# Kernel optimization log

Hardware: AMD Instinct MI355X
Metric: run time of the kernel (lower is better)

The kernel has to match this reference:

```python
import jax, jax.numpy as jnp
import numpy as np


def gat(feat_src, feat_dst, src, dst, W, al, ar, b):
    # DGL GATConv in eval mode: shared fc for src/dst, additive attention,
    # leaky_relu(0.2), edge-softmax per destination node, elu activation, bias.
    H, D = al.shape
    nd = feat_dst.shape[0]
    hs = (feat_src @ W).reshape(-1, H, D)  # [Ns,H,D]
    hd = (feat_dst @ W).reshape(-1, H, D)  # [Nd,H,D]
    el = (hs * al).sum(-1)  # [Ns,H]
    er = (hd * ar).sum(-1)  # [Nd,H]
    e = jax.nn.leaky_relu(el[src] + er[dst], 0.2)  # [E,H]
    m = jax.lax.stop_gradient(jax.ops.segment_max(e, dst, num_segments=nd))
    a = jnp.exp(e - m[dst])
    s = jax.ops.segment_sum(a, dst, num_segments=nd)
    den = s[dst]
    alpha = a / jnp.where(den == 0, 1.0, den)  # allow_zero_in_degree
    rst = jax.ops.segment_sum(alpha[:, :, None] * hs[src], dst, num_segments=nd)
    return jax.nn.elu(rst + b.reshape(H, D))  # [Nd,H,D]


def setup_inputs():
    key = jax.random.key(0)
    ks = jax.random.split(key, 40)
    NP, NQ, NK, NA = 50000, 20000, 30000, 5000
    EM, EQ, EK, EA = 1600000, 200000, 200000, 100000
    IN, ATT, HID, H, OUT = 128, 64, 32, 4, 1000
    w = lambda k, sh: jax.random.normal(k, sh, jnp.float32) * 0.05
    ri = lambda k, e, n: jax.random.randint(k, (e,), 0, n, dtype=jnp.int32)
    d = dict(
        hp=jax.random.normal(ks[0], (NP, IN), jnp.float32),
        hq=jax.random.normal(ks[1], (NQ, ATT), jnp.float32),
        hk=jax.random.normal(ks[2], (NK, ATT), jnp.float32),
        ha=jax.random.normal(ks[3], (NA, ATT), jnp.float32),
        meta_src=ri(ks[4], EM, NP), meta_dst=ri(ks[5], EM, NP),
        q_src=ri(ks[6], EQ, NQ), q_dst=ri(ks[7], EQ, NP),
        k_src=ri(ks[8], EK, NK), k_dst=ri(ks[9], EK, NP),
        a_src=ri(ks[10], EA, NA), a_dst=ri(ks[11], EA, NP),
        W0=w(ks[12], (IN, H * HID)), al0=w(ks[13], (H, HID)), ar0=w(ks[14], (H, HID)), b0=jnp.zeros((H * HID,), jnp.float32),
        W1=w(ks[15], (H * HID, H * HID)), al1=w(ks[16], (H, HID)), ar1=w(ks[17], (H, HID)), b1=jnp.zeros((H * HID,), jnp.float32),
        Wq=w(ks[18], (64, H * 128)), alq=w(ks[19], (H, 128)), arq=w(ks[20], (H, 128)), bq=jnp.zeros((H * 128,), jnp.float32),
        Wkw=w(ks[21], (64, H * 128)), alkw=w(ks[22], (H, 128)), arkw=w(ks[23], (H, 128)), bkw=jnp.zeros((H * 128,), jnp.float32),
        Watt=w(ks[24], (64, H * 128)), alatt=w(ks[25], (H, 128)), aratt=w(ks[26], (H, 128)), batt=jnp.zeros((H * 128,), jnp.float32),
        Wpnn_a=w(ks[27], (IN, 64)), Wpn_a=w(ks[28], (ATT, 64)),
        Wpnn=w(ks[29], (H * HID, 64)), Wpn=w(ks[30], (H * 128, 64)),
        Wpred=w(ks[31], (256, OUT)), bpred=jnp.zeros((OUT,), jnp.float32),
    )
    return d


def reference(hp, hq, hk, ha, meta_src, meta_dst, q_src, q_dst, k_src, k_dst, a_src, a_dst, W0, al0, ar0, b0, W1, al1, ar1, b1, Wq, alq, arq, bq, Wkw, alkw, arkw, bkw, Watt, alatt, aratt, batt, Wpnn_a, Wpn_a, Wpnn, Wpn, Wpred, bpred):
    NP = hp.shape[0]
    # two pnn_layers over the single used metapath graph (index 1 is skipped in the original)
    h = gat(hp, hp, meta_src, meta_dst, W0, al0, ar0, b0).reshape(NP, -1)  # [NP,128]
    h = gat(h, h, meta_src, meta_dst, W1, al1, ar1, b1).reshape(NP, -1)    # [NP,128]
    hpd = hp @ Wpnn_a  # proj_pnn_a(hp_cache) -> dst features for bipartite GATs
    oq = gat(hq @ Wpn_a, hpd, q_src, q_dst, Wq, alq, arq, bq).reshape(NP, -1)      # [NP,512]
    ok = gat(hk @ Wpn_a, hpd, k_src, k_dst, Wkw, alkw, arkw, bkw).reshape(NP, -1)  # [NP,512]
    oa = gat(ha @ Wpn_a, hpd, a_src, a_dst, Watt, alatt, aratt, batt).reshape(NP, -1)  # [NP,512]
    hcat = jnp.concatenate([h @ Wpnn, oq @ Wpn, ok @ Wpn, oa @ Wpn], axis=1)  # [NP,256]
    return hcat @ Wpred + bpred
```

## Files before the change

### kernel.cpp

```cpp
#include <hip/hip_runtime.h>
#include <hip/hip_bf16.h>
#include <math.h>
#include <stdint.h>

typedef __attribute__((ext_vector_type(8))) short bh8;
typedef __attribute__((ext_vector_type(4))) float f32x4;

#define AS1(p) ((const __attribute__((address_space(1))) void*)(p))
#define AS3(p) ((__attribute__((address_space(3))) void*)(p))

__device__ inline ushort f2b(float f){
  uint u = __builtin_bit_cast(uint, f);
  u += 0x7fff + ((u >> 16) & 1);
  return (ushort)(u >> 16);
}
__device__ inline float b2f(ushort b){ return __builtin_bit_cast(float, (uint)b << 16); }

__global__ void fill_zero_i32(int* __restrict__ p, int n){
  int i = blockIdx.x*blockDim.x + threadIdx.x;
  if(i < n) p[i] = 0;
}

struct P4 { const int* src; const int* dst; uint* ebuf; int E; int cap; int bbeg; int bend; };

__global__ __launch_bounds__(256) void partition_all_k(P4 g0, P4 g1, P4 g2, P4 g3,
    int* __restrict__ bcur, int range){
  P4 G; int gi;
  int b = blockIdx.x;
  if(b < g0.bend){ G = g0; gi = 0; }
  else if(b < g1.bend){ G = g1; gi = 1; }
  else if(b < g2.bend){ G = g2; gi = 2; }
  else { G = g3; gi = 3; }
  const int lb = b - G.bbeg, nb = G.bend - G.bbeg;
  __shared__ int hist[8], base[8];
  const int tid = threadIdx.x;
  int* bc = bcur + gi*8;
  for(int c0 = lb*256; c0 < G.E; c0 += nb*256){
    int i = c0 + tid;
    int d = 0, s = 0, bk = -1;
    if(i < G.E){ d = G.dst[i]; s = G.src[i]; bk = d / range; }
    if(tid < 8) hist[tid] = 0;
    __syncthreads();
    int rank = 0;
    if(bk >= 0) rank = atomicAdd(&hist[bk], 1);
    __syncthreads();
    if(tid < 8) base[tid] = hist[tid] ? atomicAdd(&bc[tid], hist[tid]) : 0;
    __syncthreads();
    if(bk >= 0){
      int pos = base[bk] + rank;
      if(pos < G.cap) G.ebuf[(size_t)bk*G.cap + pos] = ((uint)s << 13) | (uint)(d - bk*range);
    }
    __syncthreads();
  }
}

struct B4 { const uint* ebuf; int cap; int* cnt; int bbeg; int bend; };
__global__ __launch_bounds__(256) void count_all_k(B4 g0, B4 g1, B4 g2, B4 g3,
    const int* __restrict__ bcur, int range){
  B4 G; int gi;
  int b = blockIdx.x;
  if(b < g0.bend){ G = g0; gi = 0; }
  else if(b < g1.bend){ G = g1; gi = 1; }
  else if(b < g2.bend){ G = g2; gi = 2; }
  else { G = g3; gi = 3; }
  const int local = b - G.bbeg, J = (G.bend - G.bbeg) >> 3;
  const int bk = local & 7, j = local >> 3;
  int nb = bcur[gi*8 + bk]; if(nb > G.cap) nb = G.cap;
  const uint* eb = G.ebuf + (size_t)bk*G.cap;
  int* cb = G.cnt + bk*range;
  int per = (nb + J - 1)/J;
  int beg = j*per, end = beg + per; if(end > nb) end = nb;
  for(int i = beg + threadIdx.x; i < end; i += 256)
    atomicAdd(&cb[eb[i] & 8191u], 1);
}

struct SB4 { const uint* ebuf; int cap; int* cursor; int* colv; int bbeg; int bend; };
__global__ __launch_bounds__(256) void scatter_all_k(SB4 g0, SB4 g1, SB4 g2, SB4 g3,
    const int* __restrict__ bcur, int range){
  SB4 G; int gi;
  int b = blockIdx.x;
  if(b < g0.bend){ G = g0; gi = 0; }
  else if(b < g1.bend){ G = g1; gi = 1; }
  else if(b < g2.bend){ G = g2; gi = 2; }
  else { G = g3; gi = 3; }
  const int local = b - G.bbeg, J = (G.bend - G.bbeg) >> 3;
  const int bk = local & 7, j = local >> 3;
  int nb = bcur[gi*8 + bk]; if(nb > G.cap) nb = G.cap;
  const uint* eb = G.ebuf + (size_t)bk*G.cap;
  int* ub = G.cursor + bk*range;
  int per = (nb + J - 1)/J;
  int beg = j*per, end = beg + per; if(end > nb) end = nb;
  for(int i = beg + threadIdx.x; i < end; i += 256){
    uint e = eb[i];
    int p = atomicAdd(&ub[e & 8191u], 1);
    G.colv[p] = (int)(e >> 13);
  }
}

__global__ __launch_bounds__(1024) void scan4_k(
    const int* c0, const int* c1, const int* c2, const int* c3,
    int* o0, int* o1, int* o2, int* o3,
    int* u0, int* u1, int* u2, int* u3, int n){
  const int* cnt = blockIdx.x==0?c0:(blockIdx.x==1?c1:(blockIdx.x==2?c2:c3));
  int* ofs    = blockIdx.x==0?o0:(blockIdx.x==1?o1:(blockIdx.x==2?o2:o3));
  int* cursor = blockIdx.x==0?u0:(blockIdx.x==1?u1:(blockIdx.x==2?u2:u3));
  __shared__ int wsum[16];
  __shared__ int carry_s;
  int tid = threadIdx.x, wid = tid >> 6, lane = tid & 63;
  if(tid == 0) carry_s = 0;
  __syncthreads();
  for(int base = 0; base < n; base += 4096){
    int i0 = base + tid*4;
    int4 v = make_int4(0,0,0,0);
    if(i0 + 3 < n) v = *(const int4*)(cnt + i0);
    else if(i0 < n){
      v.x = cnt[i0];
      if(i0+1 < n) v.y = cnt[i0+1];
      if(i0+2 < n) v.z = cnt[i0+2];
    }
    int s1 = v.x + v.y, s2 = s1 + v.z, tot = s2 + v.w;
    int x = tot;
    #pragma unroll
    for(int off = 1; off < 64; off <<= 1){
      int t = __shfl_up(x, off);
      if(lane >= off) x += t;
    }
    if(lane == 63) wsum[wid] = x;
    __syncthreads();
    if(tid < 16){
      int y = wsum[tid];
      #pragma unroll
      for(int off = 1; off < 16; off <<= 1){
        int t = __shfl_up(y, off);
        if(tid >= off) y += t;
      }
      wsum[tid] = y;
    }
    __syncthreads();
    int pre = (wid ? wsum[wid-1] : 0) + carry_s + (x - tot);
    if(i0 + 3 < n){
      int4 o = make_int4(pre, pre+v.x, pre+s1, pre+s2);
      *(int4*)(ofs + i0) = o;
      *(int4*)(cursor + i0) = o;
    } else if(i0 < n){
      ofs[i0] = pre; cursor[i0] = pre;
      if(i0+1 < n){ ofs[i0+1] = pre+v.x; cursor[i0+1] = pre+v.x; }
      if(i0+2 < n){ ofs[i0+2] = pre+s1; cursor[i0+2] = pre+s1; }
    }
    __syncthreads();
    if(tid == 0) carry_s += wsum[15];
    __syncthreads();
  }
  if(tid == 0) ofs[n] = carry_s;
}

__global__ void cvt_all_k(const float* i0, const float* i1,
    ushort* o0, ushort* o1, int2 cum){
  int i = blockIdx.x*blockDim.x + threadIdx.x;
  const float* in; ushort* out; int base;
  if(i < cum.x){ in=i0; out=o0; base=0; }
  else if(i < cum.y){ in=i1; out=o1; base=cum.x; }
  else return;
  int l = i - base;
  float4 v = ((const float4*)in)[l];
  ushort4 o; o.x=f2b(v.x); o.y=f2b(v.y); o.z=f2b(v.z); o.w=f2b(v.w);
  ((ushort4*)out)[l] = o;
}

struct WTD { const float* W; ushort* WT; int K; int N; };
struct WTAll { WTD d[7]; int cum[8]; };
__global__ void wT_all_k(WTAll a){
  int idx = blockIdx.x*blockDim.x + threadIdx.x;
  if(idx >= a.cum[7]) return;
  int j = 0;
  #pragma unroll
  for(int t = 1; t < 7; t++) if(idx >= a.cum[t]) j = t;
  int l = idx - a.cum[j];
  WTD d = a.d[j];
  int n = l / d.K, k = l - n*d.K;
  d.WT[l] = (n < d.N) ? f2b(d.W[(size_t)k*d.N + n]) : (ushort)0;
}

__global__ void wTg3_k(const float* W0, const float* W1, const float* W2, ushort* WT){
  int idx = blockIdx.x*blockDim.x + threadIdx.x;
  if(idx >= 3*32768) return;
  int g = idx >> 15, rem = idx & 32767;
  const float* W = g==0 ? W0 : (g==1 ? W1 : W2);
  int h = rem >> 13, r2 = rem & 8191;
  int n = r2 >> 6, k = r2 & 63;
  WT[idx] = f2b(W[(size_t)k*512 + h*128 + n]);
}

struct FD { const float* W; const float* a; float* out; int K; int D; };
struct FAll { FD d[10]; };
__global__ void fold_all_k(FAll f){
  FD d = f.d[blockIdx.x];
  for(int i = threadIdx.x; i < d.K*4; i += 256){
    int k = i >> 2, h = i & 3;
    const float* wr = d.W + (size_t)k*4*d.D + (size_t)h*d.D;
    const float* ar = d.a + (size_t)h*d.D;
    float s = 0.f;
    for(int dd = 0; dd < d.D; dd++) s += wr[dd]*ar[dd];
    d.out[i] = s;
  }
}

__device__ inline void ld4v(const float* p, float* v){
  float4 t = *(const float4*)p; v[0]=t.x; v[1]=t.y; v[2]=t.z; v[3]=t.w;
}
__device__ inline void ld4v(const ushort* p, float* v){
  ushort4 t = *(const ushort4*)p; v[0]=b2f(t.x); v[1]=b2f(t.y); v[2]=b2f(t.z); v[3]=b2f(t.w);
}

__global__ __launch_bounds__(256) void gemv4v_seg3(const ushort* __restrict__ A,
    const float* __restrict__ W0, const float* __restrict__ W1, const float* __restrict__ W2,
    float* __restrict__ outv, int M, int b1, int b2){
  const int w = (blockIdx.x*blockDim.x + threadIdx.x) >> 6;
  const int lane = threadIdx.x & 63;
  const int r = lane >> 4, q = lane & 15;
  int row = w*4 + r;
  bool valid = row < M;
  int rowc = valid ? row : (M-1);
  const float* Wf = rowc < b1 ? W0 : (rowc < b2 ? W1 : W2);
  float av[4];
  ld4v(A + (size_t)rowc*64 + q*4, av);
  float a[4] = {0.f,0.f,0.f,0.f};
  #pragma unroll
  for(int kk = 0; kk < 4; kk++){
    float4 wv = *(const float4*)(Wf + (q*4+kk)*4);
    a[0] += av[kk]*wv.x; a[1] += av[kk]*wv.y; a[2] += av[kk]*wv.z; a[3] += av[kk]*wv.w;
  }
  #pragma unroll
  for(int off = 1; off < 16; off <<= 1){
    a[0] += __shfl_xor(a[0], off); a[1] += __shfl_xor(a[1], off);
    a[2] += __shfl_xor(a[2], off); a[3] += __shfl_xor(a[3], off);
  }
  if(valid && q == 0){
    float4 o; o.x=a[0]; o.y=a[1]; o.z=a[2]; o.w=a[3];
    *(float4*)(outv + (size_t)row*4) = o;
  }
}

__global__ __launch_bounds__(256) void gemv4v_er3(const ushort* __restrict__ A,
    const float* __restrict__ W0, const float* __restrict__ W1, const float* __restrict__ W2,
    float* __restrict__ o0, float* __restrict__ o1, float* __restrict__ o2, int M){
  const int w = (blockIdx.x*blockDim.x + threadIdx.x) >> 6;
  const int lane = threadIdx.x & 63;
  const int r = lane >> 4, q = lane & 15;
  int row = w*4 + r;
  bool valid = row < M;
  int rowc = valid ? row : (M-1);
  float av[4];
  ld4v(A + (size_t)rowc*64 + q*4, av);
  float a[12];
  #pragma unroll
  for(int t = 0; t < 12; t++) a[t] = 0.f;
  #pragma unroll
  for(int kk = 0; kk < 4; kk++){
    float4 w0 = *(const float4*)(W0 + (q*4+kk)*4);
    float4 w1 = *(const float4*)(W1 + (q*4+kk)*4);
    float4 w2 = *(const float4*)(W2 + (q*4+kk)*4);
    a[0] += av[kk]*w0.x; a[1] += av[kk]*w0.y; a[2] += av[kk]*w0.z; a[3] += av[kk]*w0.w;
    a[4] += av[kk]*w1.x; a[5] += av[kk]*w1.y; a[6] += av[kk]*w1.z; a[7] += av[kk]*w1.w;
    a[8] += av[kk]*w2.x; a[9] += av[kk]*w2.y; a[10]+= av[kk]*w2.z; a[11]+= av[kk]*w2.w;
  }
  #pragma unroll
  for(int off = 1; off < 16; off <<= 1)
    #pragma unroll
    for(int t = 0; t < 12; t++) a[t] += __shfl_xor(a[t], off);
  if(valid && q == 0){
    float4 x; x.x=a[0]; x.y=a[1]; x.z=a[2]; x.w=a[3];
    *(float4*)(o0 + (size_t)row*4) = x;
    float4 y; y.x=a[4]; y.y=a[5]; y.z=a[6]; y.w=a[7];
    *(float4*)(o1 + (size_t)row*4) = y;
    float4 z; z.x=a[8]; z.y=a[9]; z.z=a[10]; z.w=a[11];
    *(float4*)(o2 + (size_t)row*4) = z;
  }
}

template<typename T>
__global__ __launch_bounds__(256) void gemv8v(const T* __restrict__ A,
    const float* __restrict__ Wfa, const float* __restrict__ Wfb,
    float* __restrict__ oa, float* __restrict__ ob, int M, int lda){
  const int w = (blockIdx.x*blockDim.x + threadIdx.x) >> 6;
  const int lane = threadIdx.x & 63;
  const int r = lane >> 5, q = lane & 31;
  int row = w*2 + r;
  bool valid = row < M;
  int rowc = valid ? row : (M-1);
  float av[4];
  ld4v(A + (size_t)rowc*lda + q*4, av);
  float a[4] = {0.f,0.f,0.f,0.f}, b[4] = {0.f,0.f,0.f,0.f};
  #pragma unroll
  for(int kk = 0; kk < 4; kk++){
    float4 wa = *(const float4*)(Wfa + (q*4+kk)*4);
    float4 wb = *(const float4*)(Wfb + (q*4+kk)*4);
    a[0] += av[kk]*wa.x; a[1] += av[kk]*wa.y; a[2] += av[kk]*wa.z; a[3] += av[kk]*wa.w;
    b[0] += av[kk]*wb.x; b[1] += av[kk]*wb.y; b[2] += av[kk]*wb.z; b[3] += av[kk]*wb.w;
  }
  #pragma unroll
  for(int off = 1; off < 32; off <<= 1){
    a[0] += __shfl_xor(a[0], off); a[1] += __shfl_xor(a[1], off);
    a[2] += __shfl_xor(a[2], off); a[3] += __shfl_xor(a[3], off);
    b[0] += __shfl_xor(b[0], off); b[1] += __shfl_xor(b[1], off);
    b[2] += __shfl_xor(b[2], off); b[3] += __shfl_xor(b[3], off);
  }
  if(valid && q == 0){
    float4 o; o.x=a[0]; o.y=a[1]; o.z=a[2]; o.w=a[3];
    *(float4*)(oa + (size_t)row*4) = o;
    float4 p; p.x=b[0]; p.y=b[1]; p.z=b[2]; p.w=b[3];
    *(float4*)(ob + (size_t)row*4) = p;
  }
}

struct GSeg { const ushort* A; const ushort* BT; const float* bias; void* C; int ldc; };

template<int BN, typename OutT, bool BIAS, bool GRP, bool ELU>
__global__ __launch_bounds__(256) void gemm_mfma_b(GSeg s0, GSeg s1, GSeg s2,
    int M, int N, int K, int lda){
  constexpr int BM = 128, BK = 64;
  constexpr int NI = BN/32;
  constexpr int AIT = BM*BK/(256*8);
  constexpr int BIT = BN*BK/(256*8);
  __shared__ ushort lds[BM*BK + BN*BK];
  ushort* ldsA = lds;
  ushort* ldsB = lds + BM*BK;
  GSeg S = blockIdx.z == 0 ? s0 : (blockIdx.z == 1 ? s1 : s2);
  const int tid = threadIdx.x, wid = tid >> 6, lane = tid & 63;
  const int wr = wid >> 1, wc = wid & 1;
  const int rowbase = blockIdx.x*BM;
  const ushort* Ag = S.A;
  const ushort* Bg = S.BT;
  int colbase;
  if constexpr (GRP){
    const int hh = blockIdx.y;
    Ag = S.A + (size_t)hh*K;
    Bg = S.BT + (size_t)hh*BN*K;
    colbase = hh*BN;
  } else {
    colbase = blockIdx.y*BN;
  }

  f32x4 acc[4][NI];
  #pragma unroll
  for(int mi = 0; mi < 4; mi++)
    #pragma unroll
    for(int ni = 0; ni < NI; ni++) acc[mi][ni] = (f32x4)0.f;

  for(int k0 = 0; k0 < K; k0 += BK){
    #pragma unroll
    for(int it = 0; it < AIT; it++){
      int idx = it*256 + wid*64 + lane;
      int r = idx >> 3, sl = idx & 7;
      int kb = sl ^ (r & 7);
      int grow = rowbase + r; if(grow >= M) grow = M-1;
      const ushort* src = Ag + (size_t)grow*lda + k0 + kb*8;
      __builtin_amdgcn_global_load_lds(AS1(src), AS3(ldsA + (size_t)(it*256 + wid*64)*8), 16, 0, 0);
    }
    #pragma unroll
    for(int it = 0; it < BIT; it++){
      int idx = it*256 + wid*64 + lane;
      int r = idx >> 3, sl = idx & 7;
      int kb = sl ^ (r & 7);
      int brow = (GRP ? 0 : colbase) + r;
      const ushort* src = Bg + (size_t)brow*K + k0 + kb*8;
      __builtin_amdgcn_global_load_lds(AS1(src), AS3(ldsB + (size_t)(it*256 + wid*64)*8), 16, 0, 0);
    }
    __syncthreads();
    #pragma unroll
    for(int kk = 0; kk < 2; kk++){
      bh8 af[4], bf[NI];
      #pragma unroll
      for(int mi = 0; mi < 4; mi++){
        int arow = wr*64 + mi*16 + (lane & 15);
        int kb = kk*4 + (lane >> 4);
        af[mi] = *(const bh8*)(ldsA + arow*BK + ((kb ^ (arow & 7)) << 3));
      }
      #pragma unroll
      for(int ni = 0; ni < NI; ni++){
        int brow = wc*(BN/2) + ni*16 + (lane & 15);
        int kb = kk*4 + (lane >> 4);
        bf[ni] = *(const bh8*)(ldsB + brow*BK + ((kb ^ (brow & 7)) << 3));
      }
      #pragma unroll
      for(int mi = 0; mi < 4; mi++)
        #pragma unroll
        for(int ni = 0; ni < NI; ni++)
          acc[mi][ni] = __builtin_amdgcn_mfma_f32_16x16x32_bf16(af[mi], bf[ni], acc[mi][ni], 0, 0, 0);
    }
    __syncthreads();
  }
  OutT* C = (OutT*)S.C;
  #pragma unroll
  for(int mi = 0; mi < 4; mi++){
    #pragma unroll
    for(int ni = 0; ni < NI; ni++){
      int col = colbase + wc*(BN/2) + ni*16 + (lane & 15);
      if(col >= N) continue;
      float bv = BIAS ? S.bias[col] : 0.f;
      #pragma unroll
      for(int j = 0; j < 4; j++){
        int row = rowbase + wr*64 + mi*16 + (lane >> 4)*4 + j;
        if(row >= M) continue;
        float v = acc[mi][ni][j] + bv;
        if constexpr (ELU) v = v > 0.f ? v : (__expf(v) - 1.f);
        if constexpr (sizeof(OutT) == 4) C[(size_t)row*S.ldc + col] = v;
        else                             C[(size_t)row*S.ldc + col] = (OutT)f2b(v);
      }
    }
  }
}

__global__ __launch_bounds__(256) void gat_agg_meta(
    const ushort* __restrict__ hs, const float* __restrict__ el,
    const float* __restrict__ er, const int* __restrict__ ofs,
    const int* __restrict__ colv, const float* __restrict__ bias,
    ushort* __restrict__ outv, int Nd){
  const int wslot = threadIdx.x >> 6;
  const int node = blockIdx.x*4 + wslot;
  const int lane = threadIdx.x & 63;
  __shared__ int   lds_s[4][64];
  __shared__ float lds_w[4][256];
  if(node >= Nd) return;
  const int e0 = ofs[node], e1 = ofs[node+1];
  const int g = lane >> 4, q = lane & 15;
  const int hh = q >> 2;
  const float4 erv = *(const float4*)(er + (size_t)node*4);
  float m0=-INFINITY, m1=-INFINITY, m2=-INFINITY, m3=-INFINITY;
  float sw0=0.f, sw1=0.f, sw2=0.f, sw3=0.f;
  float acc[8];
  #pragma unroll
  for(int r = 0; r < 8; r++) acc[r] = 0.f;

  for(int base = e0; base < e1; base += 64){
    int nch = e1 - base; if(nch > 64) nch = 64;
    int s_l = colv[base + (lane < nch ? lane : nch-1)];
    float4 ev = *(const float4*)(el + (size_t)s_l*4);
    float x0 = ev.x + erv.x; x0 = x0 > 0.f ? x0 : 0.2f*x0;
    float x1 = ev.y + erv.y; x1 = x1 > 0.f ? x1 : 0.2f*x1;
    float x2 = ev.z + erv.z; x2 = x2 > 0.f ? x2 : 0.2f*x2;
    float x3 = ev.w + erv.w; x3 = x3 > 0.f ? x3 : 0.2f*x3;
    if(lane >= nch){ x0 = x1 = x2 = x3 = -INFINITY; }
    float c0=x0, c1=x1, c2=x2, c3=x3;
    #pragma unroll
    for(int off = 32; off; off >>= 1){
      c0 = fmaxf(c0, __shfl_xor(c0, off));
      c1 = fmaxf(c1, __shfl_xor(c1, off));
      c2 = fmaxf(c2, __shfl_xor(c2, off));
      c3 = fmaxf(c3, __shfl_xor(c3, off));
    }
    float n0 = fmaxf(m0,c0), n1 = fmaxf(m1,c1), n2 = fmaxf(m2,c2), n3 = fmaxf(m3,c3);
    float r0 = __expf(m0-n0), r1 = __expf(m1-n1), r2 = __expf(m2-n2), r3 = __expf(m3-n3);
    float w0 = __expf(x0-n0), w1 = __expf(x1-n1), w2 = __expf(x2-n2), w3 = __expf(x3-n3);
    sw0 = sw0*r0 + w0; sw1 = sw1*r1 + w1; sw2 = sw2*r2 + w2; sw3 = sw3*r3 + w3;
    float rh = hh==0 ? r0 : (hh==1 ? r1 : (hh==2 ? r2 : r3));
    #pragma unroll
    for(int r = 0; r < 8; r++) acc[r] *= rh;
    m0=n0; m1=n1; m2=n2; m3=n3;
    lds_s[wslot][lane] = s_l;
    lds_w[wslot][lane*4+0] = w0; lds_w[wslot][lane*4+1] = w1;
    lds_w[wslot][lane*4+2] = w2; lds_w[wslot][lane*4+3] = w3;
    int npad = (nch + 7) & ~7;
    for(int j = 0; j < npad; j += 8){
      int sA = lds_s[wslot][j + g];
      int sB = lds_s[wslot][j + 4 + g];
      float wA = lds_w[wslot][(j + g)*4 + hh];
      float wB = lds_w[wslot][(j + 4 + g)*4 + hh];
      bh8 vA = *(const bh8*)(hs + (size_t)sA*128 + q*8);
      bh8 vB = *(const bh8*)(hs + (size_t)sB*128 + q*8);
      #pragma unroll
      for(int r = 0; r < 8; r++) acc[r] += wA * b2f((ushort)vA[r]);
      #pragma unroll
      for(int r = 0; r < 8; r++) acc[r] += wB * b2f((ushort)vB[r]);
    }
  }
  #pragma unroll
  for(int off = 32; off; off >>= 1){
    sw0 += __shfl_xor(sw0, off); sw1 += __shfl_xor(sw1, off);
    sw2 += __shfl_xor(sw2, off); sw3 += __shfl_xor(sw3, off);
  }
  #pragma unroll
  for(int r = 0; r < 8; r++){
    acc[r] += __shfl_xor(acc[r], 16);
    acc[r] += __shfl_xor(acc[r], 32);
  }
  float swh = hh==0 ? sw0 : (hh==1 ? sw1 : (hh==2 ? sw2 : sw3));
  float den = (swh == 0.f) ? 1.f : swh;
  if(g == 0){
    bh8 ov;
    #pragma unroll
    for(int r = 0; r < 8; r++){
      float v = acc[r]/den + bias[q*8 + r];
      v = v > 0.f ? v : (__expf(v) - 1.f);
      ov[r] = (short)f2b(v);
    }
    *(bh8*)(outv + (size_t)node*128 + q*8) = ov;
  }
}

struct ASeg { const int* ofs; const int* colv; const float* el; const float* er; ushort* agg; };
__global__ __launch_bounds__(256) void gat_agg_proj3(ASeg s0, ASeg s1, ASeg s2,
    const ushort* __restrict__ proj, int2 pbase, int Nd, int nb){
  const int seg = blockIdx.x / nb;
  const ASeg S = seg == 0 ? s0 : (seg == 1 ? s1 : s2);
  const ushort* pj = proj + (size_t)(seg == 0 ? 0 : (seg == 1 ? pbase.x : pbase.y))*64;
  const int node = (blockIdx.x - seg*nb)*16 + (threadIdx.x >> 4);
  const int q = threadIdx.x & 15;
  if(node >= Nd) return;
  const int e0 = S.ofs[node], e1 = S.ofs[node+1];
  const float4 erv = *(const float4*)(S.er + (size_t)node*4);
  float m0=-INFINITY, m1=-INFINITY, m2=-INFINITY, m3=-INFINITY;
  for(int e = e0; e < e1; e++){
    int s = S.colv[e];
    float4 ev = *(const float4*)(S.el + (size_t)s*4);
    float x0 = ev.x + erv.x; x0 = x0 > 0.f ? x0 : 0.2f*x0;
    float x1 = ev.y + erv.y; x1 = x1 > 0.f ? x1 : 0.2f*x1;
    float x2 = ev.z + erv.z; x2 = x2 > 0.f ? x2 : 0.2f*x2;
    float x3 = ev.w + erv.w; x3 = x3 > 0.f ? x3 : 0.2f*x3;
    m0 = fmaxf(m0,x0); m1 = fmaxf(m1,x1); m2 = fmaxf(m2,x2); m3 = fmaxf(m3,x3);
  }
  float sw0=0.f, sw1=0.f, sw2=0.f, sw3=0.f;
  float acc[4][4];
  #pragma unroll
  for(int d = 0; d < 4; d++)
    #pragma unroll
    for(int h = 0; h < 4; h++) acc[d][h] = 0.f;
  for(int e = e0; e < e1; e++){
    int s = S.colv[e];
    float4 ev = *(const float4*)(S.el + (size_t)s*4);
    float x0 = ev.x + erv.x; x0 = x0 > 0.f ? x0 : 0.2f*x0;
    float x1 = ev.y + erv.y; x1 = x1 > 0.f ? x1 : 0.2f*x1;
    float x2 = ev.z + erv.z; x2 = x2 > 0.f ? x2 : 0.2f*x2;
    float x3 = ev.w + erv.w; x3 = x3 > 0.f ? x3 : 0.2f*x3;
    float w0 = __expf(x0-m0), w1 = __expf(x1-m1);
    float w2 = __expf(x2-m2), w3 = __expf(x3-m3);
    sw0 += w0; sw1 += w1; sw2 += w2; sw3 += w3;
    ushort4 p = *(const ushort4*)(pj + (size_t)s*64 + q*4);
    float f0 = b2f(p.x), f1 = b2f(p.y), f2 = b2f(p.z), f3 = b2f(p.w);
    acc[0][0] += w0*f0; acc[0][1] += w1*f0; acc[0][2] += w2*f0; acc[0][3] += w3*f0;
    acc[1][0] += w0*f1; acc[1][1] += w1*f1; acc[1][2] += w2*f1; acc[1][3] += w3*f1;
    acc[2][0] += w0*f2; acc[2][1] += w1*f2; acc[2][2] += w2*f2; acc[2][3] += w3*f2;
    acc[3][0] += w0*f3; acc[3][1] += w1*f3; acc[3][2] += w2*f3; acc[3][3] += w3*f3;
  }
  float dn[4];
  dn[0] = (sw0 == 0.f) ? 1.f : sw0;
  dn[1] = (sw1 == 0.f) ? 1.f : sw1;
  dn[2] = (sw2 == 0.f) ? 1.f : sw2;
  dn[3] = (sw3 == 0.f) ? 1.f : sw3;
  ushort* orow = S.agg + (size_t)node*256;
  #pragma unroll
  for(int h = 0; h < 4; h++){
    ushort4 o;
    o.x = f2b(acc[0][h]/dn[h]); o.y = f2b(acc[1][h]/dn[h]);
    o.z = f2b(acc[2][h]/dn[h]); o.w = f2b(acc[3][h]/dn[h]);
    *(ushort4*)(orow + h*64 + q*4) = o;
  }
}

extern "C" void kernel_launch(void* const* d_in, const int* in_sizes, int n_in,
                              void* d_out, int out_size, void* d_ws, size_t ws_size,
                              hipStream_t stream){
  const float* hp   = (const float*)d_in[0];
  const float* hq   = (const float*)d_in[1];
  const float* hk   = (const float*)d_in[2];
  const float* ha   = (const float*)d_in[3];
  const int* meta_src = (const int*)d_in[4];
  const int* meta_dst = (const int*)d_in[5];
  const int* q_src = (const int*)d_in[6];
  const int* q_dst = (const int*)d_in[7];
  const int* k_src = (const int*)d_in[8];
  const int* k_dst = (const int*)d_in[9];
  const int* a_src = (const int*)d_in[10];
  const int* a_dst = (const int*)d_in[11];
  const float* W0  = (const float*)d_in[12]; const float* al0 = (const float*)d_in[13];
  const float* ar0 = (const float*)d_in[14]; const float* b0  = (const float*)d_in[15];
  const float* W1  = (const float*)d_in[16]; const float* al1 = (const float*)d_in[17];
  const float* ar1 = (const float*)d_in[18]; const float* b1  = (const float*)d_in[19];
  const float* Wq  = (const float*)d_in[20]; const float* alq = (const float*)d_in[21];
  const float* arq = (const float*)d_in[22]; const float* bq  = (const float*)d_in[23];
  const float* Wkw = (const float*)d_in[24]; const float* alkw= (const float*)d_in[25];
  const float* arkw= (const float*)d_in[26]; const float* bkw = (const float*)d_in[27];
  const float* Watt= (const float*)d_in[28]; const float* alatt=(const float*)d_in[29];
  const float* aratt=(const float*)d_in[30]; const float* batt= (const float*)d_in[31];
  const float* Wpnn_a = (const float*)d_in[32];
  const float* Wpn_a  = (const float*)d_in[33];
  const float* Wpnn   = (const float*)d_in[34];
  const float* Wpn    = (const float*)d_in[35];
  const float* Wpred  = (const float*)d_in[36];
  const float* bpred  = (const float*)d_in[37];
  (void)n_in; (void)out_size; (void)ws_size;

  const int IN = 128, ATT = 64;
  const int NP = in_sizes[0]/IN, NQ = in_sizes[1]/ATT, NK = in_sizes[2]/ATT, NA = in_sizes[3]/ATT;
  const int EM = in_sizes[4], EQ = in_sizes[6], EK = in_sizes[8], EA = in_sizes[10];
  const int range = (NP + 7)/8;
  const int NS = NQ + NK + NA;

  uint8_t* wp = (uint8_t*)d_ws;
  auto alloc = [&](size_t bytes)->uint8_t*{
    uint8_t* p = wp; wp += (bytes + 255) & ~(size_t)255; return p;
  };
  ushort* hcat_b = (ushort*)alloc((size_t)NP*256*2);
  ushort* hbuf_b = (ushort*)alloc((size_t)NP*128*2);
  ushort* hp_b   = (ushort*)alloc((size_t)NP*128*2);
  ushort* hpd_b  = (ushort*)alloc((size_t)NP*64*2);
  ushort* hs_b   = (ushort*)alloc((size_t)NP*128*2);
  ushort* feat_all = (ushort*)alloc((size_t)NS*64*2);
  ushort* proj_all = (ushort*)alloc((size_t)NS*64*2);
  ushort* agg_all  = (ushort*)alloc((size_t)3*NP*256*2);
  ushort* o_all    = (ushort*)alloc((size_t)3*NP*512*2);
  float* el    = (float*)alloc((size_t)NP*4*4);
  float* er    = (float*)alloc((size_t)NP*4*4);
  float* el_all= (float*)alloc((size_t)NS*4*4);
  float* er_all= (float*)alloc((size_t)3*NP*4*4);
  float* wf    = (float*)alloc((size_t)10*512*4);
  int* cnt4    = (int*)alloc((size_t)(4*NP+32)*4);
  int* bcur    = cnt4 + 4*NP;
  int* cur4    = (int*)alloc((size_t)4*NP*4);
  int* ofsm    = (int*)alloc((size_t)(NP+4)*4);
  int* ofsq    = (int*)alloc((size_t)(NP+4)*4);
  int* ofsk    = (int*)alloc((size_t)(NP+4)*4);
  int* ofsa    = (int*)alloc((size_t)(NP+4)*4);
  int* colm    = (int*)alloc((size_t)EM*4);
  int* colq    = (int*)alloc((size_t)EQ*4);
  int* colk    = (int*)alloc((size_t)EK*4);
  int* cola    = (int*)alloc((size_t)EA*4);
  const int capM = EM/4+1024, capQ = EQ/4+1024, capK = EK/4+1024, capA = EA/4+1024;
  uint* ebm = (uint*)alloc((size_t)8*capM*4);
  uint* ebq = (uint*)alloc((size_t)8*capQ*4);
  uint* ebk = (uint*)alloc((size_t)8*capK*4);
  uint* eba = (uint*)alloc((size_t)8*capA*4);
  ushort* W0T    = (ushort*)alloc(128*128*2);
  ushort* W1T    = (ushort*)alloc(128*128*2);
  ushort* WTg3   = (ushort*)alloc((size_t)3*4*128*64*2);
  ushort* WpnT   = (ushort*)alloc((size_t)64*512*2);
  ushort* WpnnT  = (ushort*)alloc(64*128*2);
  ushort* Wpnn_aT= (ushort*)alloc(64*128*2);
  ushort* Wpn_aT = (ushort*)alloc(64*64*2);
  ushort* WpredT = (ushort*)alloc((size_t)1024*256*2);

  fill_zero_i32<<<(4*NP+32+255)/256, 256, 0, stream>>>(cnt4, 4*NP+32);
  {
    int bm = EM/1024 + 1, bq2 = EQ/1024 + 1, bk2 = EK/1024 + 1, ba2 = EA/1024 + 1;
    P4 g0{meta_src, meta_dst, ebm, EM, capM, 0, bm};
    P4 g1{q_src, q_dst, ebq, EQ, capQ, bm, bm+bq2};
    P4 g2{k_src, k_dst, ebk, EK, capK, bm+bq2, bm+bq2+bk2};
    P4 g3{a_src, a_dst, eba, EA, capA, bm+bq2+bk2, bm+bq2+bk2+ba2};
    partition_all_k<<<g3.bend, 256, 0, stream>>>(g0, g1, g2, g3, bcur, range);
  }
  auto Jof = [&](int E){ int J = E/65536 + 8; if(J > 48) J = 48; return J; };
  {
    int jm = 8*Jof(EM), jq = 8*Jof(EQ), jk = 8*Jof(EK), ja = 8*Jof(EA);
    B4 g0{ebm, capM, cnt4 + 0*NP, 0, jm};
    B4 g1{ebq, capQ, cnt4 + 1*NP, jm, jm+jq};
    B4 g2{ebk, capK, cnt4 + 2*NP, jm+jq, jm+jq+jk};
    B4 g3{eba, capA, cnt4 + 3*NP, jm+jq+jk, jm+jq+jk+ja};
    count_all_k<<<g3.bend, 256, 0, stream>>>(g0, g1, g2, g3, bcur, range);
    scan4_k<<<4, 1024, 0, stream>>>(cnt4, cnt4+NP, cnt4+2*NP, cnt4+3*NP,
                                    ofsm, ofsq, ofsk, ofsa,
                                    cur4, cur4+NP, cur4+2*NP, cur4+3*NP, NP);
    SB4 s0{ebm, capM, cur4 + 0*NP, colm, 0, jm};
    SB4 s1{ebq, capQ, cur4 + 1*NP, colq, jm, jm+jq};
    SB4 s2{ebk, capK, cur4 + 2*NP, colk, jm+jq, jm+jq+jk};
    SB4 s3{eba, capA, cur4 + 3*NP, cola, jm+jq+jk, jm+jq+jk+ja};
    scatter_all_k<<<s3.bend, 256, 0, stream>>>(s0, s1, s2, s3, bcur, range);
  }

  {
    int c0 = NP*128/4, c1 = c0 + NQ*64/4;
    cvt_all_k<<<(c1+255)/256, 256, 0, stream>>>(hp, hq, hp_b, feat_all, make_int2(c0, c1));
    int d0 = NK*64/4, d1 = d0 + NA*64/4;
    cvt_all_k<<<(d1+255)/256, 256, 0, stream>>>(hk, ha,
        feat_all + (size_t)NQ*64, feat_all + (size_t)(NQ+NK)*64, make_int2(d0, d1));
  }
  {
    WTAll a;
    a.d[0] = {W0, W0T, 128, 128};      a.d[1] = {W1, W1T, 128, 128};
    a.d[2] = {Wpn, WpnT, 512, 64};     a.d[3] = {Wpnn, WpnnT, 128, 64};
    a.d[4] = {Wpnn_a, Wpnn_aT, 128, 64}; a.d[5] = {Wpn_a, Wpn_aT, 64, 64};
    a.d[6] = {Wpred, WpredT, 256, 1000};
    int items[7] = {128*128, 128*128, 64*512, 64*128, 64*128, 64*64, 1024*256};
    a.cum[0] = 0;
    for(int t = 0; t < 7; t++) a.cum[t+1] = a.cum[t] + items[t];
    wT_all_k<<<(a.cum[7]+255)/256, 256, 0, stream>>>(a);
  }
  wTg3_k<<<(3*32768+255)/256, 256, 0, stream>>>(Wq, Wkw, Watt, WTg3);
  {
    FAll f;
    f.d[0] = {W0, al0, wf+0*512, 128, 32};  f.d[1] = {W0, ar0, wf+1*512, 128, 32};
    f.d[2] = {W1, al1, wf+2*512, 128, 32};  f.d[3] = {W1, ar1, wf+3*512, 128, 32};
    f.d[4] = {Wq, alq, wf+4*512, 64, 128};  f.d[5] = {Wq, arq, wf+5*512, 64, 128};
    f.d[6] = {Wkw, alkw, wf+6*512, 64, 128};f.d[7] = {Wkw, arkw, wf+7*512, 64, 128};
    f.d[8] = {Watt, alatt, wf+8*512, 64, 128};f.d[9] = {Watt, aratt, wf+9*512, 64, 128};
    fold_all_k<<<10, 256, 0, stream>>>(f);
  }

  auto launch_gemm = [&]<int BN, typename OutT, bool BIAS, bool GRP, bool ELU>(
      GSeg a, GSeg b, GSeg c, int nseg, int M, int N, int K, int lda){
    int Npad = (N + BN - 1)/BN*BN;
    dim3 g((M + 127)/128, GRP ? 4 : Npad/BN, nseg);
    gemm_mfma_b<BN, OutT, BIAS, GRP, ELU><<<g, 256, 0, stream>>>(a, b, c, M, N, K, lda);
  };
  GSeg z{};

  launch_gemm.template operator()<128, ushort, false, false, false>(
      GSeg{hp_b, W0T, nullptr, hs_b, 128}, z, z, 1, NP, 128, 128, 128);
  gemv8v<ushort><<<(NP/2+3)/4, 256, 0, stream>>>(hp_b, wf+0*512, wf+1*512, el, er, NP, 128);
  gat_agg_meta<<<(NP+3)/4, 256, 0, stream>>>(hs_b, el, er, ofsm, colm, b0, hbuf_b, NP);

  launch_gemm.template operator()<128, ushort, false, false, false>(
      GSeg{hbuf_b, W1T, nullptr, hs_b, 128}, z, z, 1, NP, 128, 128, 128);
  gemv8v<ushort><<<(NP/2+3)/4, 256, 0, stream>>>(hbuf_b, wf+2*512, wf+3*512, el, er, NP, 128);
  gat_agg_meta<<<(NP+3)/4, 256, 0, stream>>>(hs_b, el, er, ofsm, colm, b1, hbuf_b, NP);

  launch_gemm.template operator()<64, ushort, false, false, false>(
      GSeg{hbuf_b, WpnnT, nullptr, hcat_b, 256},
      GSeg{hp_b, Wpnn_aT, nullptr, hpd_b, 64}, z, 2, NP, 64, 128, 128);

  launch_gemm.template operator()<64, ushort, false, false, false>(
      GSeg{feat_all, Wpn_aT, nullptr, proj_all, 64}, z, z, 1, NS, 64, 64, 64);
  gemv4v_seg3<<<(NS/4+3)/4, 256, 0, stream>>>(proj_all, wf+4*512, wf+6*512, wf+8*512,
      el_all, NS, NQ, NQ+NK);
  gemv4v_er3<<<(NP/4+3)/4, 256, 0, stream>>>(hpd_b, wf+5*512, wf+7*512, wf+9*512,
      er_all, er_all + (size_t)NP*4, er_all + (size_t)2*NP*4, NP);
  {
    int nb = (NP+15)/16;
    ASeg a0{ofsq, colq, el_all,                    er_all,                    agg_all};
    ASeg a1{ofsk, colk, el_all + (size_t)NQ*4,     er_all + (size_t)NP*4,     agg_all + (size_t)NP*256};
    ASeg a2{ofsa, cola, el_all + (size_t)(NQ+NK)*4,er_all + (size_t)2*NP*4,   agg_all + (size_t)2*NP*256};
    gat_agg_proj3<<<3*nb, 256, 0, stream>>>(a0, a1, a2, proj_all, make_int2(NQ, NQ+NK), NP, nb);
  }
  launch_gemm.template operator()<128, ushort, true, true, true>(
      GSeg{agg_all,                    WTg3 + 0*32768, bq,   o_all, 512},
      GSeg{agg_all + (size_t)NP*256,   WTg3 + 1*32768, bkw,  o_all + (size_t)NP*512, 512},
      GSeg{agg_all + (size_t)2*NP*256, WTg3 + 2*32768, batt, o_all + (size_t)2*NP*512, 512},
      3, NP, 512, 64, 256);
  launch_gemm.template operator()<64, ushort, false, false, false>(
      GSeg{o_all,                    WpnT, nullptr, hcat_b + 64, 256},
      GSeg{o_all + (size_t)NP*512,   WpnT, nullptr, hcat_b + 128, 256},
      GSeg{o_all + (size_t)2*NP*512, WpnT, nullptr, hcat_b + 192, 256},
      3, NP, 64, 512, 512);

  launch_gemm.template operator()<128, float, true, false, false>(
      GSeg{hcat_b, WpredT, bpred, d_out, 1000}, z, z, 1, NP, 1000, 256, 256);
}
```

Measured before the change: 838.9 us.

## Fuse bipartite grouped GEMM, ELU and Wpn projection into one tail kernel

Replaces the grouped per-head GEMM with bias+ELU, which wrote a 3×NP×512 bf16 intermediate, and the following Wpn projection GEMM with a single kernel. For each 128-row tile and head, the new kernel keeps the ELU output in LDS and accumulates the 64-wide projection straight into hcat. This removes the round trip of the large o_all buffer through global memory and one launch. It also merges the two input conversion launches into one. In exchange the fused kernel uses about 80KB of LDS per block, which may limit occupancy.

```diff
diff --git a/kernel.cpp b/kernel.cpp
--- a/kernel.cpp
+++ b/kernel.cpp
@@ -154,12 +154,14 @@
   if(tid == 0) ofs[n] = carry_s;
 }
 
-__global__ void cvt_all_k(const float* i0, const float* i1,
-    ushort* o0, ushort* o1, int2 cum){
+__global__ void cvt_all_k(const float* i0, const float* i1, const float* i2, const float* i3,
+    ushort* o0, ushort* o1, ushort* o2, ushort* o3, int4 cum){
   int i = blockIdx.x*blockDim.x + threadIdx.x;
   const float* in; ushort* out; int base;
   if(i < cum.x){ in=i0; out=o0; base=0; }
   else if(i < cum.y){ in=i1; out=o1; base=cum.x; }
+  else if(i < cum.z){ in=i2; out=o2; base=cum.y; }
+  else if(i < cum.w){ in=i3; out=o3; base=cum.z; }
   else return;
   int l = i - base;
   float4 v = ((const float4*)in)[l];
@@ -315,7 +317,7 @@
 
 struct GSeg { const ushort* A; const ushort* BT; const float* bias; void* C; int ldc; };
 
-template<int BN, typename OutT, bool BIAS, bool GRP, bool ELU>
+template<int BN, typename OutT, bool BIAS>
 __global__ __launch_bounds__(256) void gemm_mfma_b(GSeg s0, GSeg s1, GSeg s2,
     int M, int N, int K, int lda){
   constexpr int BM = 128, BK = 64;
@@ -329,17 +331,7 @@
   const int tid = threadIdx.x, wid = tid >> 6, lane = tid & 63;
   const int wr = wid >> 1, wc = wid & 1;
   const int rowbase = blockIdx.x*BM;
-  const ushort* Ag = S.A;
-  const ushort* Bg = S.BT;
-  int colbase;
-  if constexpr (GRP){
-    const int hh = blockIdx.y;
-    Ag = S.A + (size_t)hh*K;
-    Bg = S.BT + (size_t)hh*BN*K;
-    colbase = hh*BN;
-  } else {
-    colbase = blockIdx.y*BN;
-  }
+  const int colbase = blockIdx.y*BN;
 
   f32x4 acc[4][NI];
   #pragma unroll
@@ -354,7 +346,7 @@
       int r = idx >> 3, sl = idx & 7;
       int kb = sl ^ (r & 7);
       int grow = rowbase + r; if(grow >= M) grow = M-1;
-      const ushort* src = Ag + (size_t)grow*lda + k0 + kb*8;
+      const ushort* src = S.A + (size_t)grow*lda + k0 + kb*8;
       __builtin_amdgcn_global_load_lds(AS1(src), AS3(ldsA + (size_t)(it*256 + wid*64)*8), 16, 0, 0);
     }
     #pragma unroll
@@ -362,8 +354,7 @@
       int idx = it*256 + wid*64 + lane;
       int r = idx >> 3, sl = idx & 7;
       int kb = sl ^ (r & 7);
-      int brow = (GRP ? 0 : colbase) + r;
-      const ushort* src = Bg + (size_t)brow*K + k0 + kb*8;
+      const ushort* src = S.BT + (size_t)(colbase + r)*K + k0 + kb*8;
       __builtin_amdgcn_global_load_lds(AS1(src), AS3(ldsB + (size_t)(it*256 + wid*64)*8), 16, 0, 0);
     }
     __syncthreads();
@@ -403,12 +394,139 @@
         int row = rowbase + wr*64 + mi*16 + (lane >> 4)*4 + j;
         if(row >= M) continue;
         float v = acc[mi][ni][j] + bv;
-        if constexpr (ELU) v = v > 0.f ? v : (__expf(v) - 1.f);
         if constexpr (sizeof(OutT) == 4) C[(size_t)row*S.ldc + col] = v;
         else                             C[(size_t)row*S.ldc + col] = (OutT)f2b(v);
       }
     }
   }
+}
+
+__global__ __launch_bounds__(256) void bip_tail_k(
+    const ushort* __restrict__ agg,
+    const ushort* __restrict__ WTg3,
+    const ushort* __restrict__ WpnT,
+    const float* bias0, const float* bias1, const float* bias2,
+    ushort* __restrict__ hcat,
+    int M){
+  __shared__ ushort ldsA[128*64];
+  __shared__ ushort ldsB[128*64];
+  __shared__ ushort ldsP[128*128];
+  __shared__ ushort ldsW[64*128];
+  const int seg = blockIdx.z;
+  const ushort* A  = agg + (size_t)seg*M*256;
+  const ushort* Wg = WTg3 + (size_t)seg*32768;
+  const float* bias = seg==0 ? bias0 : (seg==1 ? bias1 : bias2);
+  ushort* outp = hcat + 64 + seg*64;
+  const int tid = threadIdx.x, lane = tid & 63, wid = tid >> 6;
+  const int wr = wid >> 1, wc = wid & 1;
+  const int rowbase = blockIdx.x*128;
+
+  f32x4 acc_out[4][2];
+  #pragma unroll
+  for(int mi = 0; mi < 4; mi++){ acc_out[mi][0] = (f32x4)0.f; acc_out[mi][1] = (f32x4)0.f; }
+
+  for(int hh = 0; hh < 4; hh++){
+    #pragma unroll
+    for(int it = 0; it < 4; it++){
+      int idx = it*256 + tid;
+      int r = idx >> 3, sl = idx & 7;
+      int kb = sl ^ (r & 7);
+      int grow = rowbase + r; if(grow >= M) grow = M-1;
+      __builtin_amdgcn_global_load_lds(AS1(A + (size_t)grow*256 + hh*64 + kb*8),
+                                       AS3(ldsA + (size_t)idx*8), 16, 0, 0);
+    }
+    #pragma unroll
+    for(int it = 0; it < 4; it++){
+      int idx = it*256 + tid;
+      int r = idx >> 3, sl = idx & 7;
+      int kb = sl ^ (r & 7);
+      __builtin_amdgcn_global_load_lds(AS1(Wg + hh*8192 + r*64 + kb*8),
+                                       AS3(ldsB + (size_t)idx*8), 16, 0, 0);
+    }
+    #pragma unroll
+    for(int it = 0; it < 4; it++){
+      int idx = it*256 + tid;
+      int r = idx >> 4, sl = idx & 15;
+      int kb = sl ^ (r & 7);
+      __builtin_amdgcn_global_load_lds(AS1(WpnT + (size_t)r*512 + hh*128 + kb*8),
+                                       AS3(ldsW + (size_t)idx*8), 16, 0, 0);
+    }
+    __syncthreads();
+    f32x4 accp[4][4];
+    #pragma unroll
+    for(int mi = 0; mi < 4; mi++)
+      #pragma unroll
+      for(int ni = 0; ni < 4; ni++) accp[mi][ni] = (f32x4)0.f;
+    #pragma unroll
+    for(int kk = 0; kk < 2; kk++){
+      bh8 af[4], bf[4];
+      int kb = kk*4 + (lane >> 4);
+      #pragma unroll
+      for(int mi = 0; mi < 4; mi++){
+        int arow = wr*64 + mi*16 + (lane & 15);
+        af[mi] = *(const bh8*)(ldsA + arow*64 + ((kb ^ (arow & 7)) << 3));
+      }
+      #pragma unroll
+      for(int ni = 0; ni < 4; ni++){
+        int brow = wc*64 + ni*16 + (lane & 15);
+        bf[ni] = *(const bh8*)(ldsB + brow*64 + ((kb ^ (brow & 7)) << 3));
+      }
+      #pragma unroll
+      for(int mi = 0; mi < 4; mi++)
+        #pragma unroll
+        for(int ni = 0; ni < 4; ni++)
+          accp[mi][ni] = __builtin_amdgcn_mfma_f32_16x16x32_bf16(af[mi], bf[ni], accp[mi][ni], 0, 0, 0);
+    }
+    #pragma unroll
+    for(int mi = 0; mi < 4; mi++)
+      #pragma unroll
+      for(int ni = 0; ni < 4; ni++){
+        int col = wc*64 + ni*16 + (lane & 15);
+        float bv = bias[hh*128 + col];
+        int rbase = wr*64 + mi*16 + (lane >> 4)*4;
+        #pragma unroll
+        for(int j = 0; j < 4; j++){
+          float v = accp[mi][ni][j] + bv;
+          v = v > 0.f ? v : (__expf(v) - 1.f);
+          int row = rbase + j;
+          ldsP[row*128 + ((((col >> 3) ^ (row & 7))) << 3) + (col & 7)] = f2b(v);
+        }
+      }
+    __syncthreads();
+    #pragma unroll
+    for(int kk = 0; kk < 4; kk++){
+      bh8 af[4], bf[2];
+      int kb = kk*4 + (lane >> 4);
+      #pragma unroll
+      for(int mi = 0; mi < 4; mi++){
+        int arow = wr*64 + mi*16 + (lane & 15);
+        af[mi] = *(const bh8*)(ldsP + arow*128 + ((kb ^ (arow & 7)) << 3));
+      }
+      #pragma unroll
+      for(int ni = 0; ni < 2; ni++){
+        int brow = wc*32 + ni*16 + (lane & 15);
+        bf[ni] = *(const bh8*)(ldsW + brow*128 + ((kb ^ (brow & 7)) << 3));
+      }
+      #pragma unroll
+      for(int mi = 0; mi < 4; mi++)
+        #pragma unroll
+        for(int ni = 0; ni < 2; ni++)
+          acc_out[mi][ni] = __builtin_amdgcn_mfma_f32_16x16x32_bf16(af[mi], bf[ni], acc_out[mi][ni], 0, 0, 0);
+    }
+    __syncthreads();
+  }
+  #pragma unroll
+  for(int mi = 0; mi < 4; mi++)
+    #pragma unroll
+    for(int ni = 0; ni < 2; ni++){
+      int col = wc*32 + ni*16 + (lane & 15);
+      #pragma unroll
+      for(int j = 0; j < 4; j++){
+        int row = rowbase + wr*64 + mi*16 + (lane >> 4)*4 + j;
+        if(row >= M) continue;
+        outp[(size_t)row*256 + col] = f2b(acc_out[mi][ni][j]);
+      }
+    }
 }
 
 __global__ __launch_bounds__(256) void gat_agg_meta(
@@ -608,7 +726,6 @@
   ushort* feat_all = (ushort*)alloc((size_t)NS*64*2);
   ushort* proj_all = (ushort*)alloc((size_t)NS*64*2);
   ushort* agg_all  = (ushort*)alloc((size_t)3*NP*256*2);
-  ushort* o_all    = (ushort*)alloc((size_t)3*NP*512*2);
   float* el    = (float*)alloc((size_t)NP*4*4);
   float* er    = (float*)alloc((size_t)NP*4*4);
   float* el_all= (float*)alloc((size_t)NS*4*4);
@@ -667,11 +784,10 @@
   }
 
   {
-    int c0 = NP*128/4, c1 = c0 + NQ*64/4;
-    cvt_all_k<<<(c1+255)/256, 256, 0, stream>>>(hp, hq, hp_b, feat_all, make_int2(c0, c1));
-    int d0 = NK*64/4, d1 = d0 + NA*64/4;
-    cvt_all_k<<<(d1+255)/256, 256, 0, stream>>>(hk, ha,
-        feat_all + (size_t)NQ*64, feat_all + (size_t)(NQ+NK)*64, make_int2(d0, d1));
+    int c0 = NP*128/4, c1 = c0 + NQ*64/4, c2 = c1 + NK*64/4, c3 = c2 + NA*64/4;
+    cvt_all_k<<<(c3+255)/256, 256, 0, stream>>>(hp, hq, hk, ha,
+        hp_b, feat_all, feat_all + (size_t)NQ*64, feat_all + (size_t)(NQ+NK)*64,
+        make_int4(c0, c1, c2, c3));
   }
   {
     WTAll a;
@@ -695,29 +811,29 @@
     fold_all_k<<<10, 256, 0, stream>>>(f);
   }
 
-  auto launch_gemm = [&]<int BN, typename OutT, bool BIAS, bool GRP, bool ELU>(
+  auto launch_gemm = [&]<int BN, typename OutT, bool BIAS>(
       GSeg a, GSeg b, GSeg c, int nseg, int M, int N, int K, int lda){
     int Npad = (N + BN - 1)/BN*BN;
-    dim3 g((M + 127)/128, GRP ? 4 : Npad/BN, nseg);
-    gemm_mfma_b<BN, OutT, BIAS, GRP, ELU><<<g, 256, 0, stream>>>(a, b, c, M, N, K, lda);
+    dim3 g((M + 127)/128, Npad/BN, nseg);
+    gemm_mfma_b<BN, OutT, BIAS><<<g, 256, 0, stream>>>(a, b, c, M, N, K, lda);
   };
   GSeg z{};
 
-  launch_gemm.template operator()<128, ushort, false, false, false>(
+  launch_gemm.template operator()<128, ushort, false>(
       GSeg{hp_b, W0T, nullptr, hs_b, 128}, z, z, 1, NP, 128, 128, 128);
   gemv8v<ushort><<<(NP/2+3)/4, 256, 0, stream>>>(hp_b, wf+0*512, wf+1*512, el, er, NP, 128);
   gat_agg_meta<<<(NP+3)/4, 256, 0, stream>>>(hs_b, el, er, ofsm, colm, b0, hbuf_b, NP);
 
-  launch_gemm.template operator()<128, ushort, false, false, false>(
+  launch_gemm.template operator()<128, ushort, false>(
       GSeg{hbuf_b, W1T, nullptr, hs_b, 128}, z, z, 1, NP, 128, 128, 128);
   gemv8v<ushort><<<(NP/2+3)/4, 256, 0, stream>>>(hbuf_b, wf+2*512, wf+3*512, el, er, NP, 128);
   gat_agg_meta<<<(NP+3)/4, 256, 0, stream>>>(hs_b, el, er, ofsm, colm, b1, hbuf_b, NP);
 
-  launch_gemm.template operator()<64, ushort, false, false, false>(
+  launch_gemm.template operator()<64, ushort, false>(
       GSeg{hbuf_b, WpnnT, nullptr, hcat_b, 256},
       GSeg{hp_b, Wpnn_aT, nullptr, hpd_b, 64}, z, 2, NP, 64, 128, 128);
 
-  launch_gemm.template operator()<64, ushort, false, false, false>(
+  launch_gemm.template operator()<64, ushort, false>(
       GSeg{feat_all, Wpn_aT, nullptr, proj_all, 64}, z, z, 1, NS, 64, 64, 64);
   gemv4v_seg3<<<(NS/4+3)/4, 256, 0, stream>>>(proj_all, wf+4*512, wf+6*512, wf+8*512,
       el_all, NS, NQ, NQ+NK);
@@ -730,17 +846,11 @@
     ASeg a2{ofsa, cola, el_all + (size_t)(NQ+NK)*4,er_all + (size_t)2*NP*4,   agg_all + (size_t)2*NP*256};
     gat_agg_proj3<<<3*nb, 256, 0, stream>>>(a0, a1, a2, proj_all, make_int2(NQ, NQ+NK), NP, nb);
   }
-  launch_gemm.template operator()<128, ushort, true, true, true>(
-      GSeg{agg_all,                    WTg3 + 0*32768, bq,   o_all, 512},
-      GSeg{agg_all + (size_t)NP*256,   WTg3 + 1*32768, bkw,  o_all + (size_t)NP*512, 512},
-      GSeg{agg_all + (size_t)2*NP*256, WTg3 + 2*32768, batt, o_all + (size_t)2*NP*512, 512},
-      3, NP, 512, 64, 256);
-  launch_gemm.template operator()<64, ushort, false, false, false>(
-      GSeg{o_all,                    WpnT, nullptr, hcat_b + 64, 256},
-      GSeg{o_all + (size_t)NP*512,   WpnT, nullptr, hcat_b + 128, 256},
-      GSeg{o_all + (size_t)2*NP*512, WpnT, nullptr, hcat_b + 192, 256},
-      3, NP, 64, 512, 512);
-
-  launch_gemm.template operator()<128, float, true, false, false>(
+  {
+    dim3 g((NP+127)/128, 1, 3);
+    bip_tail_k<<<g, 256, 0, stream>>>(agg_all, WTg3, WpnT, bq, bkw, batt, hcat_b, NP);
+  }
+
+  launch_gemm.template operator()<128, float, true>(
       GSeg{hcat_b, WpredT, bpred, d_out, 1000}, z, z, 1, NP, 1000, 256, 256);
 }
```

Result: faster. 805.4 us (-4.0%).
